# Kernel tuning notes

Hardware: AMD Instinct MI355X
Metric: run time of the kernel (lower is better)

The kernel has to match this reference:

```python
import jax, jax.numpy as jnp
import numpy as np

EMBED = 1024
HEADS = 16
HD = EMBED // HEADS
FF = 4096
EPS = 1e-5

def _layernorm(x, g, b):
    mu = jnp.mean(x, axis=-1, keepdims=True)
    var = jnp.mean(jnp.square(x - mu), axis=-1, keepdims=True)
    return (x - mu) * jax.lax.rsqrt(var + EPS) * g + b

def setup_inputs() -> dict:
    key = jax.random.key(0)
    ks = jax.random.split(key, 10)
    s = 0.02
    return {
        "x": jax.random.normal(ks[0], (4, 2048, EMBED), dtype=jnp.float32),
        "Wq": jax.random.normal(ks[1], (EMBED, EMBED), dtype=jnp.float32) * s,
        "Wk": jax.random.normal(ks[2], (EMBED, EMBED), dtype=jnp.float32) * s,
        "Wv": jax.random.normal(ks[3], (EMBED, EMBED), dtype=jnp.float32) * s,
        "Wo": jax.random.normal(ks[4], (EMBED, EMBED), dtype=jnp.float32) * s,
        "bo": jnp.zeros((EMBED,), dtype=jnp.float32),
        "W1": jax.random.normal(ks[5], (EMBED, FF), dtype=jnp.float32) * s,
        "b1": jnp.zeros((FF,), dtype=jnp.float32),
        "W2": jax.random.normal(ks[6], (FF, EMBED), dtype=jnp.float32) * s,
        "b2": jnp.zeros((EMBED,), dtype=jnp.float32),
        "g1": jnp.ones((EMBED,), dtype=jnp.float32),
        "be1": jnp.zeros((EMBED,), dtype=jnp.float32),
        "g2": jnp.ones((EMBED,), dtype=jnp.float32),
        "be2": jnp.zeros((EMBED,), dtype=jnp.float32),
    }

def reference(x, Wq, Wk, Wv, Wo, bo, W1, b1, W2, b2, g1, be1, g2, be2):
    B, T, _ = x.shape
    # --- pre-norm self-attention (dropout = identity in eval) ---
    h = _layernorm(x, g1, be1)
    q = (h @ Wq).reshape(B, T, HEADS, HD).transpose(0, 2, 1, 3)  # bhtd
    k = (h @ Wk).reshape(B, T, HEADS, HD).transpose(0, 2, 1, 3)
    v = (h @ Wv).reshape(B, T, HEADS, HD).transpose(0, 2, 1, 3)
    scores = jnp.einsum('bhid,bhjd->bhij', q, k) / jnp.sqrt(jnp.float32(HD))
    causal = jnp.tril(jnp.ones((T, T), dtype=bool))
    scores = jnp.where(causal[None, None], scores, -jnp.inf)
    attn = jax.nn.softmax(scores, axis=-1)
    out = jnp.einsum('bhij,bhjd->bhid', attn, v)
    out = out.transpose(0, 2, 1, 3).reshape(B, T, EMBED)
    out = out @ Wo + bo
    x = x + out
    # --- pre-norm GELU FFN ---
    h2 = _layernorm(x, g2, be2)
    ff = jax.nn.gelu(h2 @ W1 + b1, approximate=False) @ W2 + b2
    return x + ff
```

## Files before the change

### kernel.cpp

```cpp
#include <hip/hip_runtime.h>

typedef unsigned short u16;
typedef __attribute__((ext_vector_type(8))) short bf16x8;
typedef __attribute__((ext_vector_type(4))) float f32x4;

#define EMBED 1024
#define FFDIM 4096
#define SEQ   2048
#define NTOK  8192
#define ATT_C 0.18033688011112042f

__device__ __forceinline__ u16 f2bf(float f) {
  union { float f; unsigned int u; } c; c.f = f;
  unsigned int r = ((c.u >> 16) & 1u) + 0x7fffu;
  return (u16)((c.u + r) >> 16);
}

__device__ __forceinline__ unsigned cvtpk(float lo, float hi) {
  unsigned r;
  asm("v_cvt_pk_bf16_f32 %0, %1, %2" : "=v"(r) : "v"(lo), "v"(hi));
  return r;
}

__device__ __forceinline__ void gload16(const u16* g, u16* l) {
  __builtin_amdgcn_global_load_lds((const __attribute__((address_space(1))) void*)g,
                                   (__attribute__((address_space(3))) void*)l, 16, 0, 0);
}

__global__ __launch_bounds__(256) void wtrans(const float* __restrict__ W,
                                              u16* __restrict__ Wt, int K, int N) {
  __shared__ float tile[32][33];
  const int tx = threadIdx.x & 31, ty = threadIdx.x >> 5;
  const int n0 = blockIdx.x << 5, k0 = blockIdx.y << 5;
#pragma unroll
  for (int r = 0; r < 32; r += 8)
    tile[ty + r][tx] = W[(size_t)(k0 + ty + r) * N + n0 + tx];
  __syncthreads();
#pragma unroll
  for (int r = 0; r < 32; r += 8)
    Wt[(size_t)(n0 + ty + r) * K + k0 + tx] = f2bf(tile[tx][ty + r]);
}

__global__ __launch_bounds__(256) void vtrans(const u16* __restrict__ qkv,
                                              u16* __restrict__ Vt) {
  __shared__ u16 tile[32][33];
  const int tx = threadIdx.x & 31, ty = threadIdx.x >> 5;
  const int t0 = blockIdx.x << 5;
  const int rg0 = blockIdx.y << 5;
  const int bh = rg0 >> 6, d0 = rg0 & 63;
  const int b = bh >> 4, h = bh & 15;
#pragma unroll
  for (int r = 0; r < 32; r += 8)
    tile[ty + r][tx] = qkv[(size_t)(b * SEQ + t0 + ty + r) * 3072 + 2048 + h * 64 + d0 + tx];
  __syncthreads();
#pragma unroll
  for (int r = 0; r < 32; r += 8)
    Vt[(size_t)(rg0 + ty + r) * SEQ + t0 + tx] = tile[tx][ty + r];
}

__global__ __launch_bounds__(256) void ln_kernel(const float* __restrict__ xin,
                                                 const float* __restrict__ gamma,
                                                 const float* __restrict__ beta,
                                                 u16* __restrict__ out) {
  const int row = blockIdx.x, tid = threadIdx.x;
  const float4 v = reinterpret_cast<const float4*>(xin + (size_t)row * EMBED)[tid];
  float s  = v.x + v.y + v.z + v.w;
  float ss = v.x * v.x + v.y * v.y + v.z * v.z + v.w * v.w;
#pragma unroll
  for (int m = 1; m < 64; m <<= 1) { s += __shfl_xor(s, m); ss += __shfl_xor(ss, m); }
  __shared__ float red[8];
  if ((tid & 63) == 0) { red[tid >> 6] = s; red[4 + (tid >> 6)] = ss; }
  __syncthreads();
  s  = red[0] + red[1] + red[2] + red[3];
  ss = red[4] + red[5] + red[6] + red[7];
  const float mean = s * (1.0f / EMBED);
  const float var  = ss * (1.0f / EMBED) - mean * mean;
  const float rstd = rsqrtf(var + 1e-5f);
  const float4 g  = reinterpret_cast<const float4*>(gamma)[tid];
  const float4 bb = reinterpret_cast<const float4*>(beta)[tid];
  ushort4 o;
  o.x = f2bf((v.x - mean) * rstd * g.x + bb.x);
  o.y = f2bf((v.y - mean) * rstd * g.y + bb.y);
  o.z = f2bf((v.z - mean) * rstd * g.z + bb.z);
  o.w = f2bf((v.w - mean) * rstd * g.w + bb.w);
  reinterpret_cast<ushort4*>(out + (size_t)row * EMBED)[tid] = o;
}

template <int NREP, int EPI>
__global__ __launch_bounds__(512, 2) void gemm7(const u16* __restrict__ A,
                                                const u16* __restrict__ Bt,
                                                void* __restrict__ Cv,
                                                const float* __restrict__ bias,
                                                const float* __restrict__ res,
                                                int M, int N, int K) {
  constexpr int BN = NREP * 64;
  constexpr int VH = (NREP == 4) ? 6 : 4;
  __shared__ __align__(16) u16 As[2][256 * 64];
  __shared__ __align__(16) u16 Bs[2][BN * 64];

  const int tid = threadIdx.x;
  const int lane = tid & 63, wid = tid >> 6;
  const int l4 = lane >> 4, l15 = lane & 15;
  const int wq = wid >> 2, wn = wid & 3;

  const int gx = gridDim.x;
  const int nwg = gx * (int)gridDim.y;
  const int flat = (int)blockIdx.y * gx + (int)blockIdx.x;
  const int cpx = nwg >> 3;
  const int swz = (flat & 7) * cpx + (flat >> 3);
  const int brow = (swz / gx) << 8;
  const int bcol = (swz % gx) * BN;

  const f32x4 z4 = {0.f, 0.f, 0.f, 0.f};
  f32x4 acc[4][4][NREP / 2];
#pragma unroll
  for (int q = 0; q < 4; ++q)
#pragma unroll
    for (int m = 0; m < 4; ++m)
#pragma unroll
      for (int n = 0; n < NREP / 2; ++n) acc[q][m][n] = z4;

  const int srow = tid >> 3;
  const int scolb = ((tid & 7) << 4) ^ ((srow & 7) << 4);
  const u16* gAs = A  + (size_t)(brow + srow) * K + (scolb >> 1);
  const u16* gBs = Bt + (size_t)(bcol + srow) * K + (scolb >> 1);
  const int lA = wid * 512;

  const int nk = K >> 6;

#define STAGE_A(c_, t_, h_)                                                     \
  do {                                                                          \
    gload16(gAs + (size_t)((h_) * 128) * K + (size_t)(t_) * 64,                 \
            &As[c_][(h_) * 8192 + lA]);                                         \
    gload16(gAs + (size_t)((h_) * 128 + 64) * K + (size_t)(t_) * 64,            \
            &As[c_][(h_) * 8192 + 4096 + lA]);                                  \
  } while (0)
#define STAGE_B(c_, t_, h_)                                                     \
  do {                                                                          \
    if constexpr (NREP == 4) {                                                  \
      gload16(gBs + (size_t)((h_) * 128) * K + (size_t)(t_) * 64,               \
              &Bs[c_][(h_) * 8192 + lA]);                                       \
      gload16(gBs + (size_t)((h_) * 128 + 64) * K + (size_t)(t_) * 64,          \
              &Bs[c_][(h_) * 8192 + 4096 + lA]);                                \
    } else {                                                                    \
      gload16(gBs + (size_t)((h_) * 64) * K + (size_t)(t_) * 64,                \
              &Bs[c_][(h_) * 4096 + lA]);                                       \
    }                                                                           \
  } while (0)

  const int kk0  = l4 << 3;
  const int aswz = (l15 & 7) << 3;

#define RD_A(MH)                                                                \
  _Pragma("unroll")                                                             \
  for (int m_ = 0; m_ < 4; ++m_)                                                \
    _Pragma("unroll")                                                           \
    for (int ks_ = 0; ks_ < 2; ++ks_)                                           \
      af[m_][ks_] = *(const bf16x8*)&As[c][((MH) * 128 + wq * 64 + m_ * 16 + l15) * 64 + ((kk0 + ks_ * 32) ^ aswz)];
#define RD_B(DST, NH)                                                           \
  _Pragma("unroll")                                                             \
  for (int n_ = 0; n_ < NREP / 2; ++n_)                                         \
    _Pragma("unroll")                                                           \
    for (int ks_ = 0; ks_ < 2; ++ks_)                                           \
      DST[n_][ks_] = *(const bf16x8*)&Bs[c][((NH) * (BN / 2) + wn * (BN / 8) + n_ * 16 + l15) * 64 + ((kk0 + ks_ * 32) ^ aswz)];
#define GATE_LG                                                                 \
  __builtin_amdgcn_s_barrier();                                                 \
  asm volatile("s_waitcnt lgkmcnt(0)" ::: "memory");                            \
  __builtin_amdgcn_sched_barrier(0)
#define VM(N_) asm volatile("s_waitcnt vmcnt(%0)" :: "i"(N_) : "memory")
#define MFMA_Q(Q_, BF_)                                                         \
  _Pragma("unroll")                                                             \
  for (int m_ = 0; m_ < 4; ++m_)                                                \
    _Pragma("unroll")                                                           \
    for (int n_ = 0; n_ < NREP / 2; ++n_)                                       \
      _Pragma("unroll")                                                         \
      for (int ks_ = 0; ks_ < 2; ++ks_)                                         \
        acc[Q_][m_][n_] = __builtin_amdgcn_mfma_f32_16x16x32_bf16(              \
            af[m_][ks_], BF_[n_][ks_], acc[Q_][m_][n_], 0, 0, 0);

  bf16x8 af[4][2], bf0[NREP / 2][2], bf1[NREP / 2][2];

  STAGE_A(0, 0, 0);
  STAGE_B(0, 0, 0);
  STAGE_B(0, 0, 1);
  STAGE_A(0, 0, 1);
  VM(2);
  __builtin_amdgcn_s_barrier();

  for (int t = 0; t < nk; ++t) {
    const int c = t & 1, cn = c ^ 1;
    RD_A(0); RD_B(bf0, 0); RD_B(bf1, 1);
    if (t + 1 < nk) { STAGE_B(cn, t + 1, 0); STAGE_B(cn, t + 1, 1); STAGE_A(cn, t + 1, 0); }
    GATE_LG;
    __builtin_amdgcn_s_setprio(1);
    MFMA_Q(0, bf0);
    MFMA_Q(1, bf1);
    __builtin_amdgcn_s_setprio(0);
    __builtin_amdgcn_s_barrier();
    if (t + 1 < nk) { VM(VH); } else { VM(0); }
    RD_A(1);
    if (t + 1 < nk) STAGE_A(cn, t + 1, 1);
    GATE_LG;
    __builtin_amdgcn_s_setprio(1);
    MFMA_Q(2, bf1);
    MFMA_Q(3, bf0);
    __builtin_amdgcn_s_setprio(0);
    VM(2);
    __builtin_amdgcn_s_barrier();
  }

#undef STAGE_A
#undef STAGE_B
#undef RD_A
#undef RD_B
#undef GATE_LG
#undef VM
#undef MFMA_Q

#pragma unroll
  for (int q = 0; q < 4; ++q) {
    const int mh = q >> 1, nh = (q >> 1) ^ (q & 1);
    const int rowb = brow + mh * 128 + wq * 64 + (l4 << 2);
    const int colb = bcol + nh * (BN / 2) + wn * (BN / 8) + l15;
#pragma unroll
    for (int n = 0; n < NREP / 2; ++n) {
      const int col = colb + n * 16;
      float bv = 0.f;
      if (EPI != 0) bv = bias[col];
#pragma unroll
      for (int m = 0; m < 4; ++m) {
#pragma unroll
        for (int j = 0; j < 4; ++j) {
          const int row = rowb + m * 16 + j;
          const float v = acc[q][m][n][j];
          if (EPI == 0) {
            ((u16*)Cv)[(size_t)row * N + col] = f2bf(v);
          } else if (EPI == 1) {
            ((float*)Cv)[(size_t)row * N + col] = v + bv + res[(size_t)row * N + col];
          } else {
            const float t2 = v + bv;
            const float gl = 0.5f * t2 * (1.0f + erff(t2 * 0.70710678118654752f));
            ((u16*)Cv)[(size_t)row * N + col] = f2bf(gl);
          }
        }
      }
    }
  }
}

__global__ __launch_bounds__(512) void attn_fwd(const u16* __restrict__ qkv,
                                                const u16* __restrict__ Vt,
                                                u16* __restrict__ attn) {
  __shared__ __align__(16) u16 Ks[64 * 72];
  __shared__ __align__(16) u16 Vs[64 * 72];
  __shared__ __align__(16) u16 Ps[8 * 16 * 72];
  const int tid = threadIdx.x, lane = tid & 63, wid = tid >> 6;
  const int l4 = lane >> 4, l15 = lane & 15;
  const int bh = blockIdx.y, b = bh >> 4, h = bh & 15;
  const size_t bt0 = (size_t)b * SEQ;
  u16* Pw = &Ps[wid * 16 * 72];

  const int sr = tid >> 3;
  const int sc0 = (tid & 7) << 3;
  const u16* kbase = qkv + bt0 * 3072 + 1024 + h * 64;
  const u16* vbase = Vt + (size_t)bh * 64 * SEQ;
  const f32x4 z4 = {0.f, 0.f, 0.f, 0.f};

#pragma unroll
  for (int ph = 0; ph < 2; ++ph) {
    const int Qb = ((ph == 0) ? (int)blockIdx.x : 15 - (int)blockIdx.x) << 7;
    const int qw = Qb + wid * 16;
    const int qlane = qw + l15;

    const u16* qp = qkv + (bt0 + qlane) * 3072 + h * 64 + (l4 << 3);
    const bf16x8 aq0 = *(const bf16x8*)qp;
    const bf16x8 aq1 = *(const bf16x8*)(qp + 32);

    f32x4 o[4];
#pragma unroll
    for (int dt = 0; dt < 4; ++dt) o[dt] = z4;
    float mrun = -1e30f, lrun = 0.f;

    bf16x8 kp = *(const bf16x8*)(kbase + (size_t)sr * 3072 + sc0);
    bf16x8 vp = *(const bf16x8*)(vbase + (size_t)sr * SEQ + sc0);

    const int jend = Qb + 128;
    for (int j0 = 0; j0 < jend; j0 += 64) {
      __syncthreads();
      *(bf16x8*)&Ks[sr * 72 + sc0] = kp;
      *(bf16x8*)&Vs[sr * 72 + sc0] = vp;
      __syncthreads();

      if (j0 + 64 < jend) {
        kp = *(const bf16x8*)(kbase + (size_t)(j0 + 64 + sr) * 3072 + sc0);
        vp = *(const bf16x8*)(vbase + (size_t)sr * SEQ + j0 + 64 + sc0);
      }

      if (j0 > qw + 15) continue;
      const int nt = min(4, ((qw + 15 - j0) >> 4) + 1);

      f32x4 s[4];
#pragma unroll
      for (int t = 0; t < 4; ++t) {
        if (t < nt) {
          const bf16x8 ak0 = *(const bf16x8*)&Ks[(t * 16 + l15) * 72 + (l4 << 3)];
          const bf16x8 ak1 = *(const bf16x8*)&Ks[(t * 16 + l15) * 72 + 32 + (l4 << 3)];
          f32x4 a = z4;
          a = __builtin_amdgcn_mfma_f32_16x16x32_bf16(ak0, aq0, a, 0, 0, 0);
          a = __builtin_amdgcn_mfma_f32_16x16x32_bf16(ak1, aq1, a, 0, 0, 0);
          s[t] = a;
        }
      }

      float mt = -1e30f;
#pragma unroll
      for (int t = 0; t < 4; ++t) {
        if (t < nt) {
          if (j0 + t * 16 + 15 > qw) {
            const int kvb = j0 + t * 16 + (l4 << 2);
#pragma unroll
            for (int j = 0; j < 4; ++j)
              if (kvb + j > qlane) s[t][j] = -1e30f;
          }
          mt = fmaxf(mt, fmaxf(fmaxf(s[t][0], s[t][1]), fmaxf(s[t][2], s[t][3])));
        }
      }
      mt = fmaxf(mt, __shfl_xor(mt, 16));
      mt = fmaxf(mt, __shfl_xor(mt, 32));

      const bool skip = __all(mt <= mrun + 44.0f);
      float scq = 1.0f;
      if (!skip) {
        const float mn = fmaxf(mrun, mt);
        scq = exp2f((mrun - mn) * ATT_C);
        mrun = mn;
      }
      const float mc = mrun * ATT_C;

      float ls = 0.f;
      uint2 pw[4];
#pragma unroll
      for (int t = 0; t < 4; ++t) {
        if (t < nt) {
          const float p0 = exp2f(__builtin_fmaf(s[t][0], ATT_C, -mc));
          const float p1 = exp2f(__builtin_fmaf(s[t][1], ATT_C, -mc));
          const float p2 = exp2f(__builtin_fmaf(s[t][2], ATT_C, -mc));
          const float p3 = exp2f(__builtin_fmaf(s[t][3], ATT_C, -mc));
          ls += (p0 + p1) + (p2 + p3);
          pw[t].x = cvtpk(p0, p1);
          pw[t].y = cvtpk(p2, p3);
        } else {
          pw[t].x = 0u; pw[t].y = 0u;
        }
      }
#pragma unroll
      for (int t = 0; t < 4; ++t)
        *(uint2*)&Pw[l15 * 72 + t * 16 + (l4 << 2)] = pw[t];

      ls += __shfl_xor(ls, 16);
      ls += __shfl_xor(ls, 32);

      if (!skip) {
        lrun = lrun * scq + ls;
#pragma unroll
        for (int dt = 0; dt < 4; ++dt)
#pragma unroll
          for (int j = 0; j < 4; ++j) o[dt][j] *= scq;
      } else {
        lrun += ls;
      }

      const int nc = (nt + 1) >> 1;
#pragma unroll
      for (int c = 0; c < 2; ++c) {
        if (c < nc) {
          const bf16x8 ap = *(const bf16x8*)&Pw[l15 * 72 + c * 32 + (l4 << 3)];
#pragma unroll
          for (int dt = 0; dt < 4; ++dt) {
            const bf16x8 bv = *(const bf16x8*)&Vs[(dt * 16 + l15) * 72 + c * 32 + (l4 << 3)];
            o[dt] = __builtin_amdgcn_mfma_f32_16x16x32_bf16(bv, ap, o[dt], 0, 0, 0);
          }
        }
      }
    }

    const float rl = 1.0f / lrun;
#pragma unroll
    for (int dt = 0; dt < 4; ++dt) {
      uint2 w;
      w.x = cvtpk(o[dt][0] * rl, o[dt][1] * rl);
      w.y = cvtpk(o[dt][2] * rl, o[dt][3] * rl);
      *(uint2*)&Pw[l15 * 72 + dt * 16 + (l4 << 2)] = w;
    }
#pragma unroll
    for (int rep = 0; rep < 2; ++rep) {
      const int unit = rep * 64 + lane;
      const int r = unit >> 3, c = unit & 7;
      const bf16x8 v = *(const bf16x8*)&Pw[r * 72 + c * 8];
      *(bf16x8*)&attn[(bt0 + qw + r) * EMBED + h * 64 + c * 8] = v;
    }
  }
}

extern "C" void kernel_launch(void* const* d_in, const int* in_sizes, int n_in,
                              void* d_out, int out_size, void* d_ws, size_t ws_size,
                              hipStream_t stream) {
  const float* x   = (const float*)d_in[0];
  const float* Wq  = (const float*)d_in[1];
  const float* Wk  = (const float*)d_in[2];
  const float* Wv  = (const float*)d_in[3];
  const float* Wo  = (const float*)d_in[4];
  const float* bo  = (const float*)d_in[5];
  const float* W1  = (const float*)d_in[6];
  const float* b1  = (const float*)d_in[7];
  const float* W2  = (const float*)d_in[8];
  const float* b2  = (const float*)d_in[9];
  const float* g1  = (const float*)d_in[10];
  const float* be1 = (const float*)d_in[11];
  const float* g2  = (const float*)d_in[12];
  const float* be2 = (const float*)d_in[13];

  char* ws = (char*)d_ws;
  u16* wqkv_t = (u16*)(ws + 0);
  u16* wo_t   = (u16*)(ws + 6291456);
  u16* w1_t   = (u16*)(ws + 8388608);
  u16* w2_t   = (u16*)(ws + 16777216);
  u16* hbuf   = (u16*)(ws + 25165824);
  u16* qkv    = (u16*)(ws + 41943040);
  u16* ff1    = (u16*)(ws + 41943040);
  u16* vt     = (u16*)(ws + 92274688);
  u16* attnb  = (u16*)(ws + 109051904);
  float* x2   = (float*)(ws + 125829120);
  float* outp = (float*)d_out;

  dim3 blk(256);
  wtrans<<<dim3(32, 32),  blk, 0, stream>>>(Wq, wqkv_t,               1024, 1024);
  wtrans<<<dim3(32, 32),  blk, 0, stream>>>(Wk, wqkv_t + 1024 * 1024, 1024, 1024);
  wtrans<<<dim3(32, 32),  blk, 0, stream>>>(Wv, wqkv_t + 2048 * 1024, 1024, 1024);
  wtrans<<<dim3(32, 32),  blk, 0, stream>>>(Wo, wo_t,                 1024, 1024);
  wtrans<<<dim3(128, 32), blk, 0, stream>>>(W1, w1_t,                 1024, 4096);
  wtrans<<<dim3(32, 128), blk, 0, stream>>>(W2, w2_t,                 4096, 1024);

  ln_kernel<<<dim3(8192), blk, 0, stream>>>(x, g1, be1, hbuf);
  gemm7<2, 0><<<dim3(24, 32), dim3(512), 0, stream>>>(hbuf, wqkv_t, qkv, nullptr, nullptr,
                                                      8192, 3072, 1024);
  vtrans<<<dim3(64, 128), blk, 0, stream>>>(qkv, vt);
  attn_fwd<<<dim3(8, 64), dim3(512), 0, stream>>>(qkv, vt, attnb);
  gemm7<2, 1><<<dim3(8, 32), dim3(512), 0, stream>>>(attnb, wo_t, x2, bo, x,
                                                     8192, 1024, 1024);
  ln_kernel<<<dim3(8192), blk, 0, stream>>>(x2, g2, be2, hbuf);
  gemm7<4, 2><<<dim3(16, 32), dim3(512), 0, stream>>>(hbuf, w1_t, ff1, b1, nullptr,
                                                      8192, 4096, 1024);
  gemm7<2, 1><<<dim3(8, 32), dim3(512), 0, stream>>>(ff1, w2_t, outp, b2, x2,
                                                     8192, 1024, 4096);
}
```

Before: 414.2 us.

## Shrink attention blocks to 4 waves with swizzled grid; merge QKVO weight transposes

```diff
diff --git a/kernel.cpp b/kernel.cpp
--- a/kernel.cpp
+++ b/kernel.cpp
@@ -39,6 +39,34 @@
 #pragma unroll
   for (int r = 0; r < 32; r += 8)
     Wt[(size_t)(n0 + ty + r) * K + k0 + tx] = f2bf(tile[tx][ty + r]);
+}
+
+__global__ __launch_bounds__(256) void wtrans4(const float* __restrict__ Wq,
+                                               const float* __restrict__ Wk,
+                                               const float* __restrict__ Wv,
+                                               const float* __restrict__ Wo,
+                                               u16* __restrict__ o0,
+                                               u16* __restrict__ o1,
+                                               u16* __restrict__ o2,
+                                               u16* __restrict__ o3) {
+  __shared__ float tile[32][33];
+  const float* W;
+  u16* Wt;
+  switch (blockIdx.z) {
+    case 0: W = Wq; Wt = o0; break;
+    case 1: W = Wk; Wt = o1; break;
+    case 2: W = Wv; Wt = o2; break;
+    default: W = Wo; Wt = o3; break;
+  }
+  const int tx = threadIdx.x & 31, ty = threadIdx.x >> 5;
+  const int n0 = blockIdx.x << 5, k0 = blockIdx.y << 5;
+#pragma unroll
+  for (int r = 0; r < 32; r += 8)
+    tile[ty + r][tx] = W[(size_t)(k0 + ty + r) * 1024 + n0 + tx];
+  __syncthreads();
+#pragma unroll
+  for (int r = 0; r < 32; r += 8)
+    Wt[(size_t)(n0 + ty + r) * 1024 + k0 + tx] = f2bf(tile[tx][ty + r]);
 }
 
 __global__ __launch_bounds__(256) void vtrans(const u16* __restrict__ qkv,
@@ -248,27 +276,31 @@
   }
 }
 
-__global__ __launch_bounds__(512) void attn_fwd(const u16* __restrict__ qkv,
+__global__ __launch_bounds__(256) void attn_fwd(const u16* __restrict__ qkv,
                                                 const u16* __restrict__ Vt,
                                                 u16* __restrict__ attn) {
   __shared__ __align__(16) u16 Ks[64 * 72];
   __shared__ __align__(16) u16 Vs[64 * 72];
-  __shared__ __align__(16) u16 Ps[8 * 16 * 72];
+  __shared__ __align__(16) u16 Ps[4 * 16 * 72];
   const int tid = threadIdx.x, lane = tid & 63, wid = tid >> 6;
   const int l4 = lane >> 4, l15 = lane & 15;
-  const int bh = blockIdx.y, b = bh >> 4, h = bh & 15;
+  const int d = (int)blockIdx.y * 16 + (int)blockIdx.x;
+  const int L = (d & 7) * 128 + (d >> 3);
+  const int p = L & 15, bh = L >> 4;
+  const int b = bh >> 4, h = bh & 15;
   const size_t bt0 = (size_t)b * SEQ;
   u16* Pw = &Ps[wid * 16 * 72];
 
-  const int sr = tid >> 3;
-  const int sc0 = (tid & 7) << 3;
+  const int sr = tid >> 2;
+  const int sc0 = (tid & 3) << 4;
   const u16* kbase = qkv + bt0 * 3072 + 1024 + h * 64;
   const u16* vbase = Vt + (size_t)bh * 64 * SEQ;
   const f32x4 z4 = {0.f, 0.f, 0.f, 0.f};
 
 #pragma unroll
   for (int ph = 0; ph < 2; ++ph) {
-    const int Qb = ((ph == 0) ? (int)blockIdx.x : 15 - (int)blockIdx.x) << 7;
+    const int tj = (ph == 0) ? p : 31 - p;
+    const int Qb = tj << 6;
     const int qw = Qb + wid * 16;
     const int qlane = qw + l15;
 
@@ -281,19 +313,26 @@
     for (int dt = 0; dt < 4; ++dt) o[dt] = z4;
     float mrun = -1e30f, lrun = 0.f;
 
-    bf16x8 kp = *(const bf16x8*)(kbase + (size_t)sr * 3072 + sc0);
-    bf16x8 vp = *(const bf16x8*)(vbase + (size_t)sr * SEQ + sc0);
-
-    const int jend = Qb + 128;
+    bf16x8 kp0 = *(const bf16x8*)(kbase + (size_t)sr * 3072 + sc0);
+    bf16x8 kp1 = *(const bf16x8*)(kbase + (size_t)sr * 3072 + sc0 + 8);
+    bf16x8 vp0 = *(const bf16x8*)(vbase + (size_t)sr * SEQ + sc0);
+    bf16x8 vp1 = *(const bf16x8*)(vbase + (size_t)sr * SEQ + sc0 + 8);
+
+    const int jend = Qb + 64;
     for (int j0 = 0; j0 < jend; j0 += 64) {
       __syncthreads();
-      *(bf16x8*)&Ks[sr * 72 + sc0] = kp;
-      *(bf16x8*)&Vs[sr * 72 + sc0] = vp;
+      *(bf16x8*)&Ks[sr * 72 + sc0]     = kp0;
+      *(bf16x8*)&Ks[sr * 72 + sc0 + 8] = kp1;
+      *(bf16x8*)&Vs[sr * 72 + sc0]     = vp0;
+      *(bf16x8*)&Vs[sr * 72 + sc0 + 8] = vp1;
       __syncthreads();
 
       if (j0 + 64 < jend) {
-        kp = *(const bf16x8*)(kbase + (size_t)(j0 + 64 + sr) * 3072 + sc0);
-        vp = *(const bf16x8*)(vbase + (size_t)sr * SEQ + j0 + 64 + sc0);
+        const size_t kro = (size_t)(j0 + 64 + sr);
+        kp0 = *(const bf16x8*)(kbase + kro * 3072 + sc0);
+        kp1 = *(const bf16x8*)(kbase + kro * 3072 + sc0 + 8);
+        vp0 = *(const bf16x8*)(vbase + (size_t)sr * SEQ + j0 + 64 + sc0);
+        vp1 = *(const bf16x8*)(vbase + (size_t)sr * SEQ + j0 + 64 + sc0 + 8);
       }
 
       if (j0 > qw + 15) continue;
@@ -434,18 +473,17 @@
   float* outp = (float*)d_out;
 
   dim3 blk(256);
-  wtrans<<<dim3(32, 32),  blk, 0, stream>>>(Wq, wqkv_t,               1024, 1024);
-  wtrans<<<dim3(32, 32),  blk, 0, stream>>>(Wk, wqkv_t + 1024 * 1024, 1024, 1024);
-  wtrans<<<dim3(32, 32),  blk, 0, stream>>>(Wv, wqkv_t + 2048 * 1024, 1024, 1024);
-  wtrans<<<dim3(32, 32),  blk, 0, stream>>>(Wo, wo_t,                 1024, 1024);
-  wtrans<<<dim3(128, 32), blk, 0, stream>>>(W1, w1_t,                 1024, 4096);
-  wtrans<<<dim3(32, 128), blk, 0, stream>>>(W2, w2_t,                 4096, 1024);
+  wtrans4<<<dim3(32, 32, 4), blk, 0, stream>>>(Wq, Wk, Wv, Wo,
+                                               wqkv_t, wqkv_t + 1024 * 1024,
+                                               wqkv_t + 2048 * 1024, wo_t);
+  wtrans<<<dim3(128, 32), blk, 0, stream>>>(W1, w1_t, 1024, 4096);
+  wtrans<<<dim3(32, 128), blk, 0, stream>>>(W2, w2_t, 4096, 1024);
 
   ln_kernel<<<dim3(8192), blk, 0, stream>>>(x, g1, be1, hbuf);
   gemm7<2, 0><<<dim3(24, 32), dim3(512), 0, stream>>>(hbuf, wqkv_t, qkv, nullptr, nullptr,
                                                       8192, 3072, 1024);
   vtrans<<<dim3(64, 128), blk, 0, stream>>>(qkv, vt);
-  attn_fwd<<<dim3(8, 64), dim3(512), 0, stream>>>(qkv, vt, attnb);
+  attn_fwd<<<dim3(16, 64), blk, 0, stream>>>(qkv, vt, attnb);
   gemm7<2, 1><<<dim3(8, 32), dim3(512), 0, stream>>>(attnb, wo_t, x2, bo, x,
                                                      8192, 1024, 1024);
   ln_kernel<<<dim3(8192), blk, 0, stream>>>(x2, g2, be2, hbuf);
```

Result: slower. 426.8 us (+3.1%).
